# Optimization experiments

Measured on AMD Instinct MI355X. Metric: run time of the kernel, lower is better.

The kernel has to match this reference:

```python
import jax, jax.numpy as jnp
import numpy as np

G = 100000   # num graphs
N = 2000000  # num nodes
E = 4000000  # num edges (unused downstream, kept for fidelity)
D = 300      # emb_dim
L = 50       # num noise levels


def setup_inputs() -> dict:
    key = jax.random.key(0)
    ks = jax.random.split(key, 12)
    node2graph = jnp.sort(jax.random.randint(ks[0], (N,), 0, G))
    edge_index = jax.random.randint(ks[1], (2, E), 0, N)
    noise_level = jax.random.randint(ks[2], (G,), 0, L)
    molecule_repr = jax.random.normal(ks[3], (G, D), dtype=jnp.float32)
    pos_noise_pred = jax.random.normal(ks[4], (N, 3), dtype=jnp.float32)
    pos_perturbed = jax.random.normal(ks[5], (N, 3), dtype=jnp.float32)
    pos_target = jax.random.normal(ks[6], (N, 3), dtype=jnp.float32)
    s = 1.0 / np.sqrt(D)
    W1 = jax.random.uniform(ks[7], (D, D), minval=-s, maxval=s, dtype=jnp.float32)
    b1 = jax.random.uniform(ks[8], (D,), minval=-s, maxval=s, dtype=jnp.float32)
    W2 = jax.random.uniform(ks[9], (D, D), minval=-s, maxval=s, dtype=jnp.float32)
    b2 = jax.random.uniform(ks[10], (D,), minval=-s, maxval=s, dtype=jnp.float32)
    sigmas = jnp.asarray(np.exp(np.linspace(np.log(10.0), np.log(0.01), L)), dtype=jnp.float32)
    return dict(node2graph=node2graph, edge_index=edge_index, noise_level=noise_level,
                num_graphs=G, molecule_repr=molecule_repr, pos_noise_pred=pos_noise_pred,
                pos_perturbed=pos_perturbed, pos_target=pos_target,
                W1=W1, b1=b1, W2=W2, b2=b2, sigmas=sigmas)


def _score_target_riemann(pos_perturbed, pos_target, node2graph, num_graphs):
    # @torch.no_grad() branch: all scatter_mean/scatter_add indexed by node2graph
    seg_sum = lambda x: jax.ops.segment_sum(x, node2graph, num_segments=num_graphs)
    cnt = jnp.maximum(seg_sum(jnp.ones((node2graph.shape[0],), jnp.float32)), 1.0)[:, None]
    center = seg_sum(pos_target) / cnt                 # [G,3]
    p_center = seg_sum(pos_perturbed) / cnt            # [G,3]
    pos_c = pos_target - center[node2graph]            # [N,3]
    pp_c = pos_perturbed - p_center[node2graph]        # [N,3]
    # per-graph 3x3 matrices: ptp[i,j] = sum pp_i*pp_j, otp[i,j] = sum pos_c_i*pp_j
    ptp = seg_sum(pp_c[:, :, None] * pp_c[:, None, :])   # [G,3,3]
    otp = seg_sum(pos_c[:, :, None] * pp_c[:, None, :])  # [G,3,3]
    ptp_n = ptp[node2graph]                              # [N,3,3]
    otp_n = otp[node2graph]                              # [N,3,3]
    num = -2.0 * (jnp.einsum('ni,nij->nj', pp_c, ptp_n)
                  - jnp.einsum('ni,nij->nj', pos_c, otp_n))  # [N,3]
    den = (jnp.linalg.norm(ptp_n.reshape(-1, 9), axis=-1)
           + jnp.linalg.norm(otp_n.reshape(-1, 9), axis=-1))[:, None]
    return num / den


def reference(node2graph, edge_index, noise_level, num_graphs, molecule_repr,
              pos_noise_pred, pos_perturbed, pos_target, W1, b1, W2, b2, sigmas):
    edge2graph = node2graph[edge_index[0]]  # computed but unused, as in original
    used_sigmas = sigmas[noise_level][node2graph][:, None]  # [N,1]
    score_target = jax.lax.stop_gradient(
        _score_target_riemann(pos_perturbed, pos_target, node2graph, num_graphs)
    ) / used_sigmas
    pred_noise = (pos_noise_pred - pos_perturbed) * (1.0 / used_sigmas)
    per_node = jnp.sum((pred_noise - score_target) ** 2, axis=-1)  # [N]
    per_graph = jax.ops.segment_sum(per_node, node2graph, num_segments=num_graphs)
    pos_denoise = per_graph.mean()
    # noise-level prediction head: Linear -> SiLU -> Linear, CE over noise_level
    h = jax.nn.silu(molecule_repr @ W1 + b1)
    logits = h @ W2 + b2  # [G,D]
    logp = jax.nn.log_softmax(logits, axis=-1)
    ce = -jnp.take_along_axis(logp, noise_level[:, None], axis=1)[:, 0]
    loss_pred_noise = ce.mean()
    return jnp.stack([pos_denoise, loss_pred_noise])
```

## Files before the change

kernel.cpp:

```cpp
#include <hip/hip_runtime.h>
#include <math.h>


typedef __attribute__((ext_vector_type(8))) short bf16x8;
typedef __attribute__((ext_vector_type(4))) short s16x4;
typedef __attribute__((ext_vector_type(4))) float f32x4;

__device__ __forceinline__ short bt(float f) {
    return (short)(__float_as_uint(f) >> 16);
}

#define TM   32
#define DRL  300
#define DP   320
#define XS   328
#define NT   20
#define NW   5
#define KCH  10


#define NB_PREPW 800

__global__ __launch_bounds__(256)
void k_prep(const float* __restrict__ W1, const float* __restrict__ W2,
            short* __restrict__ Wb1, short* __restrict__ Wb2,
            const int* __restrict__ n2g, int* __restrict__ gs,
            int* __restrict__ ge, int N) {
    const int bid = blockIdx.x;
    const int tid = threadIdx.x;
    if (bid < NB_PREPW) {
        int id = bid * 256 + tid;
        int mat = id / (DP * DP);
        int rem = id - mat * DP * DP;
        int k = rem / DP, n = rem - (rem / DP) * DP;
        const float* W = mat ? W2 : W1;
        short* Wb = mat ? Wb2 : Wb1;
        float v = (k < DRL && n < DRL) ? W[k * DRL + n] : 0.f;
        int kc = k >> 5, kin = k & 31, quad = kin >> 3, j = kin & 7;
        int t = n >> 4, l16 = n & 15;
        Wb[(((kc * NT + t) * 64) + quad * 16 + l16) * 8 + j] = bt(v);
    } else {
        int t = (bid - NB_PREPW) * 256 + tid;
        if (t < N) {
            int g = n2g[t];
            if (t == 0     || n2g[t - 1] != g) gs[g] = t;
            if (t == N - 1 || n2g[t + 1] != g) ge[g] = t + 1;
        }
    }
}


__global__ __launch_bounds__(256, 4)
void k_main(const int* __restrict__ gs, const int* __restrict__ ge,
            const float* __restrict__ pt, const float* __restrict__ pp,
            const float* __restrict__ pnp,
            const int* __restrict__ nl, const float* __restrict__ sigmas,
            double* __restrict__ accA,
            const float* __restrict__ X,
            const short* __restrict__ Wb1, const short* __restrict__ Wb2,
            const float* __restrict__ b1, const float* __restrict__ b2,
            double* __restrict__ accC, int G) {
    __shared__ __align__(16) short Xs[TM * XS];

    const int bid = blockIdx.x;
    const int tid = threadIdx.x;
    const int t3  = bid / 3;
    const int r3  = bid - t3 * 3;

    if (r3 == 0) {
        const int tg = t3 * 256 + tid;
        const int g  = tg >> 2;
        const int j  = tg & 3;
        float q = 0.f;
        if (g < G) {
            const int s = gs[g], e = ge[g];
            const int g0 = s >> 2, g1 = (e + 3) >> 2;
            const float4* ptv = (const float4*)pt;
            const float4* ppv = (const float4*)pp;
            const float4* pnv = (const float4*)pnp;
            float st0=0,st1=0,st2=0, sp0=0,sp1=0,sp2=0;
            float m00=0,m01=0,m02=0,m11=0,m12=0,m22=0;
            float t00=0,t01=0,t02=0,t10=0,t11=0,t12=0,t20=0,t21=0,t22=0;
            for (int gg = g0 + j; gg < g1; gg += 4) {
                float4 x0 = ptv[3*gg], x1 = ptv[3*gg+1], x2 = ptv[3*gg+2];
                float4 y0 = ppv[3*gg], y1 = ppv[3*gg+1], y2 = ppv[3*gg+2];
                float A[12] = {x0.x,x0.y,x0.z,x0.w, x1.x,x1.y,x1.z,x1.w,
                               x2.x,x2.y,x2.z,x2.w};
                float B[12] = {y0.x,y0.y,y0.z,y0.w, y1.x,y1.y,y1.z,y1.w,
                               y2.x,y2.y,y2.z,y2.w};
                const int base = gg * 4;
#pragma unroll
                for (int k = 0; k < 4; ++k) {
                    const int i = base + k;
                    const bool v = (i >= s) && (i < e);
                    float a0 = v ? A[3*k+0] : 0.f;
                    float a1 = v ? A[3*k+1] : 0.f;
                    float a2 = v ? A[3*k+2] : 0.f;
                    float b0 = v ? B[3*k+0] : 0.f;
                    float b1v = v ? B[3*k+1] : 0.f;
                    float b2v = v ? B[3*k+2] : 0.f;
                    st0 += a0; st1 += a1; st2 += a2;
                    sp0 += b0; sp1 += b1v; sp2 += b2v;
                    m00 += b0*b0;  m01 += b0*b1v;  m02 += b0*b2v;
                    m11 += b1v*b1v; m12 += b1v*b2v; m22 += b2v*b2v;
                    t00 += a0*b0; t01 += a0*b1v; t02 += a0*b2v;
                    t10 += a1*b0; t11 += a1*b1v; t12 += a1*b2v;
                    t20 += a2*b0; t21 += a2*b1v; t22 += a2*b2v;
                }
            }
#define QR(x) do { x += __shfl_xor(x, 1, 64); x += __shfl_xor(x, 2, 64); } while (0)
            QR(st0); QR(st1); QR(st2); QR(sp0); QR(sp1); QR(sp2);
            QR(m00); QR(m01); QR(m02); QR(m11); QR(m12); QR(m22);
            QR(t00); QR(t01); QR(t02); QR(t10); QR(t11); QR(t12);
            QR(t20); QR(t21); QR(t22);
#undef QR
            float cnt = fmaxf((float)(e - s), 1.f);
            float ic  = 1.f / cnt;
            float c0 = st0 * ic, c1 = st1 * ic, c2 = st2 * ic;
            float d0 = sp0 * ic, d1 = sp1 * ic, d2 = sp2 * ic;
            float p00 = m00 - cnt*d0*d0, p01 = m01 - cnt*d0*d1;
            float p02 = m02 - cnt*d0*d2, p11 = m11 - cnt*d1*d1;
            float p12 = m12 - cnt*d1*d2, p22 = m22 - cnt*d2*d2;
            float o00 = t00 - cnt*c0*d0, o01 = t01 - cnt*c0*d1, o02 = t02 - cnt*c0*d2;
            float o10 = t10 - cnt*c1*d0, o11 = t11 - cnt*c1*d1, o12 = t12 - cnt*c1*d2;
            float o20 = t20 - cnt*c2*d0, o21 = t21 - cnt*c2*d1, o22 = t22 - cnt*c2*d2;
            float ptn = sqrtf(p00*p00 + p11*p11 + p22*p22 +
                              2.f*(p01*p01 + p02*p02 + p12*p12));
            float otn = sqrtf(o00*o00 + o01*o01 + o02*o02 +
                              o10*o10 + o11*o11 + o12*o12 +
                              o20*o20 + o21*o21 + o22*o22);
            float den = ptn + otn;
            float idn = (den > 0.f) ? (1.f / den) : 0.f;
            float sg  = sigmas[nl[g]];
            float is2 = 1.f / (sg * sg);
            for (int gg = g0 + j; gg < g1; gg += 4) {
                float4 x0 = ptv[3*gg], x1 = ptv[3*gg+1], x2 = ptv[3*gg+2];
                float4 y0 = ppv[3*gg], y1 = ppv[3*gg+1], y2 = ppv[3*gg+2];
                float4 z0 = pnv[3*gg], z1 = pnv[3*gg+1], z2 = pnv[3*gg+2];
                float A[12] = {x0.x,x0.y,x0.z,x0.w, x1.x,x1.y,x1.z,x1.w,
                               x2.x,x2.y,x2.z,x2.w};
                float B[12] = {y0.x,y0.y,y0.z,y0.w, y1.x,y1.y,y1.z,y1.w,
                               y2.x,y2.y,y2.z,y2.w};
                float C[12] = {z0.x,z0.y,z0.z,z0.w, z1.x,z1.y,z1.z,z1.w,
                               z2.x,z2.y,z2.z,z2.w};
                const int base = gg * 4;
#pragma unroll
                for (int k = 0; k < 4; ++k) {
                    const int i = base + k;
                    const bool v = (i >= s) && (i < e);
                    float a0 = A[3*k+0] - c0, a1 = A[3*k+1] - c1, a2 = A[3*k+2] - c2;
                    float bb0 = B[3*k+0], bb1 = B[3*k+1], bb2 = B[3*k+2];
                    float b0 = bb0 - d0, b1v = bb1 - d1, b2v = bb2 - d2;
                    float n0 = -2.f * ((b0*p00 + b1v*p01 + b2v*p02) - (a0*o00 + a1*o10 + a2*o20));
                    float n1 = -2.f * ((b0*p01 + b1v*p11 + b2v*p12) - (a0*o01 + a1*o11 + a2*o21));
                    float n2 = -2.f * ((b0*p02 + b1v*p12 + b2v*p22) - (a0*o02 + a1*o12 + a2*o22));
                    float e0 = (C[3*k+0] - bb0) - n0 * idn;
                    float e1 = (C[3*k+1] - bb1) - n1 * idn;
                    float e2 = (C[3*k+2] - bb2) - n2 * idn;
                    float contrib = (e0*e0 + e1*e1 + e2*e2) * is2;
                    q += v ? contrib : 0.f;
                }
            }
        }
        for (int o = 32; o > 0; o >>= 1) q += __shfl_down(q, o, 64);
        if ((tid & 63) == 0)
            atomicAdd(&accA[(t3 * 4 + (tid >> 6)) & 255], (double)q);
        return;
    }

    const int mid = t3 * 2 + (r3 - 1);
    const int wv   = tid >> 6;
    const int lane = tid & 63;
    const int quad = lane >> 4;
    const int l16  = lane & 15;
    const int m0   = mid * TM;
    const int tb0  = wv * NW;

    const float4* Xv = (const float4*)X;
    for (int idx = tid; idx < TM * 75; idx += 256) {
        int r = idx / 75, c = idx - r * 75;
        int gr = m0 + r;
        float4 v = {0.f, 0.f, 0.f, 0.f};
        if (gr < G) v = Xv[gr * 75 + c];
        s16x4 sv = { bt(v.x), bt(v.y), bt(v.z), bt(v.w) };
        *(s16x4*)&Xs[r * XS + c * 4] = sv;
    }
    for (int idx = tid; idx < TM * (DP - DRL); idx += 256) {
        int r = idx / (DP - DRL), c = idx - r * (DP - DRL);
        Xs[r * XS + DRL + c] = 0;
    }
    __syncthreads();

    const bf16x8* B1 = (const bf16x8*)Wb1;
    const bf16x8* B2 = (const bf16x8*)Wb2;

    f32x4 acc[2][NW];
    const f32x4 vzero = {0.f, 0.f, 0.f, 0.f};
#pragma unroll
    for (int m = 0; m < 2; ++m)
#pragma unroll
        for (int n = 0; n < NW; ++n) acc[m][n] = vzero;

#pragma unroll
    for (int kc = 0; kc < KCH; ++kc) {
        bf16x8 bv[NW];
#pragma unroll
        for (int n = 0; n < NW; ++n) bv[n] = B1[(kc * NT + tb0 + n) * 64 + lane];
        bf16x8 a0 = *(const bf16x8*)&Xs[(l16) * XS + kc * 32 + quad * 8];
        bf16x8 a1 = *(const bf16x8*)&Xs[(16 + l16) * XS + kc * 32 + quad * 8];
#pragma unroll
        for (int n = 0; n < NW; ++n) {
            acc[0][n] = __builtin_amdgcn_mfma_f32_16x16x32_bf16(a0, bv[n], acc[0][n], 0, 0, 0);
            acc[1][n] = __builtin_amdgcn_mfma_f32_16x16x32_bf16(a1, bv[n], acc[1][n], 0, 0, 0);
        }
    }
    __syncthreads();

#pragma unroll
    for (int n = 0; n < NW; ++n) {
        int col = (tb0 + n) * 16 + l16;
        float bias = (col < DRL) ? b1[col] : 0.f;
#pragma unroll
        for (int m = 0; m < 2; ++m)
#pragma unroll
            for (int r = 0; r < 4; ++r) {
                float v = acc[m][n][r] + bias;
                float h = v / (1.f + __expf(-v));
                Xs[(m * 16 + quad * 4 + r) * XS + col] = bt(h);
            }
    }
    __syncthreads();

#pragma unroll
    for (int m = 0; m < 2; ++m)
#pragma unroll
        for (int n = 0; n < NW; ++n) acc[m][n] = vzero;
#pragma unroll
    for (int kc = 0; kc < KCH; ++kc) {
        bf16x8 bv[NW];
#pragma unroll
        for (int n = 0; n < NW; ++n) bv[n] = B2[(kc * NT + tb0 + n) * 64 + lane];
        bf16x8 a0 = *(const bf16x8*)&Xs[(l16) * XS + kc * 32 + quad * 8];
        bf16x8 a1 = *(const bf16x8*)&Xs[(16 + l16) * XS + kc * 32 + quad * 8];
#pragma unroll
        for (int n = 0; n < NW; ++n) {
            acc[0][n] = __builtin_amdgcn_mfma_f32_16x16x32_bf16(a0, bv[n], acc[0][n], 0, 0, 0);
            acc[1][n] = __builtin_amdgcn_mfma_f32_16x16x32_bf16(a1, bv[n], acc[1][n], 0, 0, 0);
        }
    }
    __syncthreads();

    float* S = (float*)Xs;
    float* T = S + TM * 4;
#pragma unroll
    for (int m = 0; m < 2; ++m) {
#pragma unroll
        for (int r = 0; r < 4; ++r) {
            int row = m * 16 + quad * 4 + r;
            int grow = m0 + row;
            int ct = (grow < G) ? nl[grow] : -1;
            float sw = 0.f;
#pragma unroll
            for (int n = 0; n < NW; ++n) {
                int col = (tb0 + n) * 16 + l16;
                float lg = acc[m][n][r] + ((col < DRL) ? b2[col] : 0.f);
                if (col < DRL) sw += __expf(lg);
                if (col == ct) T[row] = lg;
            }
            for (int o = 1; o < 16; o <<= 1) sw += __shfl_xor(sw, o, 64);
            if (l16 == 0) S[row * 4 + wv] = sw;
        }
    }
    __syncthreads();
    if (tid < 64) {
        float q = 0.f;
        int row = tid;
        if (row < TM) {
            int grow = m0 + row;
            if (grow < G) {
                float ss = S[row*4+0] + S[row*4+1] + S[row*4+2] + S[row*4+3];
                q = __logf(ss) - T[row];
            }
        }
        for (int o = 32; o > 0; o >>= 1) q += __shfl_down(q, o, 64);
        if (tid == 0) atomicAdd(&accC[mid & 255], (double)q);
    }
}


__global__ void k_final(const double* __restrict__ accA,
                        const double* __restrict__ accC,
                        float* __restrict__ out, float invG) {
    int t = threadIdx.x;
    double a = accA[t] + accA[t + 64] + accA[t + 128] + accA[t + 192];
    double c = accC[t] + accC[t + 64] + accC[t + 128] + accC[t + 192];
    for (int o = 32; o > 0; o >>= 1) {
        a += __shfl_down(a, o, 64);
        c += __shfl_down(c, o, 64);
    }
    if (t == 0) {
        out[0] = (float)(a * (double)invG);
        out[1] = (float)(c * (double)invG);
    }
}


extern "C" void kernel_launch(void* const* d_in, const int* in_sizes, int n_in,
                              void* d_out, int out_size, void* d_ws, size_t ws_size,
                              hipStream_t stream) {
    const int*   n2g = (const int*)d_in[0];
    const int*   nl  = (const int*)d_in[2];
    const float* X   = (const float*)d_in[4];
    const float* pnp = (const float*)d_in[5];
    const float* pp  = (const float*)d_in[6];
    const float* pt  = (const float*)d_in[7];
    const float* W1  = (const float*)d_in[8];
    const float* b1  = (const float*)d_in[9];
    const float* W2  = (const float*)d_in[10];
    const float* b2  = (const float*)d_in[11];
    const float* sig = (const float*)d_in[12];

    const int N = in_sizes[0];
    const int G = in_sizes[2];

    double* accA = (double*)d_ws;
    double* accC = accA + 256;
    short*  Wb1  = (short*)((char*)d_ws + 4096);
    short*  Wb2  = Wb1 + DP * DP;
    int*    gs   = (int*)((char*)d_ws + 4096 + (size_t)2 * DP * DP * 2);
    int*    ge   = gs + G;

    hipMemsetAsync(d_ws, 0, 4096, stream);
    hipMemsetAsync(gs, 0, (size_t)2 * G * 4, stream);

    const int nb_bnd = (N + 255) / 256;
    const int nbg    = (4 * G + 255) / 256;
    const int nmain  = 3 * nbg;

    k_prep<<<NB_PREPW + nb_bnd, 256, 0, stream>>>(W1, W2, Wb1, Wb2,
                                                  n2g, gs, ge, N);
    k_main<<<nmain, 256, 0, stream>>>(gs, ge, pt, pp, pnp, nl, sig, accA,
                                      X, Wb1, Wb2, b1, b2, accC, G);
    k_final<<<1, 64, 0, stream>>>(accA, accC, (float*)d_out, 1.0f / (float)G);
}
```

Measured before the change: 358.7 us.

## Fuse finalize into main kernel, binary-search graph bounds, pre-convert X to bf16

Drops the two memsets and the separate final kernel. Zeroing of the accumulators moves into the prep kernel, and the final reduction is done by the last block of the main kernel through an atomic ticket. Graph start and end offsets are now found by a binary search over the sorted node2graph in the main kernel, replacing the boundary-scan pass. X is also pre-converted to padded bf16 in the prep kernel when the workspace is large enough. This cuts launches and the extra memory pass, at the cost of per-thread log(N) searches and an extra write and read of X in bf16.

```diff
diff --git a/kernel.cpp b/kernel.cpp
--- a/kernel.cpp
+++ b/kernel.cpp
@@ -17,15 +17,14 @@
 #define NT   20
 #define NW   5
 #define KCH  10
-
-
 #define NB_PREPW 800
+
 
 __global__ __launch_bounds__(256)
 void k_prep(const float* __restrict__ W1, const float* __restrict__ W2,
             short* __restrict__ Wb1, short* __restrict__ Wb2,
-            const int* __restrict__ n2g, int* __restrict__ gs,
-            int* __restrict__ ge, int N) {
+            const float* __restrict__ X, short* __restrict__ Xb,
+            double* __restrict__ accZ, int G, int nxb) {
     const int bid = blockIdx.x;
     const int tid = threadIdx.x;
     if (bid < NB_PREPW) {
@@ -39,28 +38,37 @@
         int kc = k >> 5, kin = k & 31, quad = kin >> 3, j = kin & 7;
         int t = n >> 4, l16 = n & 15;
         Wb[(((kc * NT + t) * 64) + quad * 16 + l16) * 8 + j] = bt(v);
+    } else if (bid < NB_PREPW + nxb) {
+        int id = (bid - NB_PREPW) * 256 + tid;
+        if (id < G * 80) {
+            int row = id / 80, grp = id - (id / 80) * 80;
+            float4 v = {0.f, 0.f, 0.f, 0.f};
+            if (grp < 75) v = ((const float4*)X)[row * 75 + grp];
+            s16x4 sv = { bt(v.x), bt(v.y), bt(v.z), bt(v.w) };
+            ((s16x4*)Xb)[row * 80 + grp] = sv;
+        }
     } else {
-        int t = (bid - NB_PREPW) * 256 + tid;
-        if (t < N) {
-            int g = n2g[t];
-            if (t == 0     || n2g[t - 1] != g) gs[g] = t;
-            if (t == N - 1 || n2g[t + 1] != g) ge[g] = t + 1;
-        }
+        accZ[tid] = 0.0;
+        accZ[256 + tid] = 0.0;
+        if (tid == 0) ((unsigned int*)&accZ[512])[0] = 0u;
     }
 }
 
 
 __global__ __launch_bounds__(256, 4)
-void k_main(const int* __restrict__ gs, const int* __restrict__ ge,
+void k_main(const int* __restrict__ n2g,
             const float* __restrict__ pt, const float* __restrict__ pp,
             const float* __restrict__ pnp,
             const int* __restrict__ nl, const float* __restrict__ sigmas,
-            double* __restrict__ accA,
-            const float* __restrict__ X,
+            const float* __restrict__ X, const short* __restrict__ Xb,
             const short* __restrict__ Wb1, const short* __restrict__ Wb2,
             const float* __restrict__ b1, const float* __restrict__ b2,
-            double* __restrict__ accC, int G) {
+            double* __restrict__ accA, double* __restrict__ accC,
+            unsigned int* __restrict__ ticket, float* __restrict__ out,
+            float invG, int G, int N, int nblocks, int useXb) {
     __shared__ __align__(16) short Xs[TM * XS];
+    __shared__ int lastBlk;
+    __shared__ double ax[4], cx[4];
 
     const int bid = blockIdx.x;
     const int tid = threadIdx.x;
@@ -71,9 +79,18 @@
         const int tg = t3 * 256 + tid;
         const int g  = tg >> 2;
         const int j  = tg & 3;
+        const int lane = tid & 63;
         float q = 0.f;
         if (g < G) {
-            const int s = gs[g], e = ge[g];
+            int target = g + (j & 1);
+            int lo = 0, hi = N;
+            while (lo < hi) {
+                int mid = (int)(((unsigned)lo + (unsigned)hi) >> 1);
+                if (n2g[mid] < target) lo = mid + 1; else hi = mid;
+            }
+            const int qb = lane & ~3;
+            const int s = __shfl(lo, qb + 0, 64);
+            const int e = __shfl(lo, qb + 1, 64);
             const int g0 = s >> 2, g1 = (e + 3) >> 2;
             const float4* ptv = (const float4*)pt;
             const float4* ppv = (const float4*)pp;
@@ -163,144 +180,167 @@
             }
         }
         for (int o = 32; o > 0; o >>= 1) q += __shfl_down(q, o, 64);
-        if ((tid & 63) == 0)
+        if ((tid & 63) == 0) {
             atomicAdd(&accA[(t3 * 4 + (tid >> 6)) & 255], (double)q);
-        return;
+            __threadfence();
+        }
+    } else {
+        const int mid = t3 * 2 + (r3 - 1);
+        const int wv   = tid >> 6;
+        const int lane = tid & 63;
+        const int quad = lane >> 4;
+        const int l16  = lane & 15;
+        const int m0   = mid * TM;
+        const int tb0  = wv * NW;
+
+        if (useXb) {
+            const bf16x8* Xbv = (const bf16x8*)Xb;
+#pragma unroll
+            for (int u = 0; u < 5; ++u) {
+                int idx = tid + u * 256;
+                int r = idx / 40, c8 = idx - (idx / 40) * 40;
+                int gr = m0 + r;
+                bf16x8 v = (bf16x8){0,0,0,0,0,0,0,0};
+                if (gr < G) v = Xbv[gr * 40 + c8];
+                *(bf16x8*)&Xs[r * XS + c8 * 8] = v;
+            }
+        } else {
+            const float4* Xv = (const float4*)X;
+            for (int idx = tid; idx < TM * 75; idx += 256) {
+                int r = idx / 75, c = idx - r * 75;
+                int gr = m0 + r;
+                float4 v = {0.f, 0.f, 0.f, 0.f};
+                if (gr < G) v = Xv[gr * 75 + c];
+                s16x4 sv = { bt(v.x), bt(v.y), bt(v.z), bt(v.w) };
+                *(s16x4*)&Xs[r * XS + c * 4] = sv;
+            }
+            for (int idx = tid; idx < TM * (DP - DRL); idx += 256) {
+                int r = idx / (DP - DRL), c = idx - r * (DP - DRL);
+                Xs[r * XS + DRL + c] = 0;
+            }
+        }
+        __syncthreads();
+
+        const bf16x8* B1 = (const bf16x8*)Wb1;
+        const bf16x8* B2 = (const bf16x8*)Wb2;
+
+        f32x4 acc[2][NW];
+        const f32x4 vzero = {0.f, 0.f, 0.f, 0.f};
+#pragma unroll
+        for (int m = 0; m < 2; ++m)
+#pragma unroll
+            for (int n = 0; n < NW; ++n) acc[m][n] = vzero;
+
+#pragma unroll
+        for (int kc = 0; kc < KCH; ++kc) {
+            bf16x8 bv[NW];
+#pragma unroll
+            for (int n = 0; n < NW; ++n) bv[n] = B1[(kc * NT + tb0 + n) * 64 + lane];
+            bf16x8 a0 = *(const bf16x8*)&Xs[(l16) * XS + kc * 32 + quad * 8];
+            bf16x8 a1 = *(const bf16x8*)&Xs[(16 + l16) * XS + kc * 32 + quad * 8];
+#pragma unroll
+            for (int n = 0; n < NW; ++n) {
+                acc[0][n] = __builtin_amdgcn_mfma_f32_16x16x32_bf16(a0, bv[n], acc[0][n], 0, 0, 0);
+                acc[1][n] = __builtin_amdgcn_mfma_f32_16x16x32_bf16(a1, bv[n], acc[1][n], 0, 0, 0);
+            }
+        }
+        __syncthreads();
+
+#pragma unroll
+        for (int n = 0; n < NW; ++n) {
+            int col = (tb0 + n) * 16 + l16;
+            float bias = (col < DRL) ? b1[col] : 0.f;
+#pragma unroll
+            for (int m = 0; m < 2; ++m)
+#pragma unroll
+                for (int r = 0; r < 4; ++r) {
+                    float v = acc[m][n][r] + bias;
+                    float h = v / (1.f + __expf(-v));
+                    Xs[(m * 16 + quad * 4 + r) * XS + col] = bt(h);
+                }
+        }
+        __syncthreads();
+
+#pragma unroll
+        for (int m = 0; m < 2; ++m)
+#pragma unroll
+            for (int n = 0; n < NW; ++n) acc[m][n] = vzero;
+#pragma unroll
+        for (int kc = 0; kc < KCH; ++kc) {
+            bf16x8 bv[NW];
+#pragma unroll
+            for (int n = 0; n < NW; ++n) bv[n] = B2[(kc * NT + tb0 + n) * 64 + lane];
+            bf16x8 a0 = *(const bf16x8*)&Xs[(l16) * XS + kc * 32 + quad * 8];
+            bf16x8 a1 = *(const bf16x8*)&Xs[(16 + l16) * XS + kc * 32 + quad * 8];
+#pragma unroll
+            for (int n = 0; n < NW; ++n) {
+                acc[0][n] = __builtin_amdgcn_mfma_f32_16x16x32_bf16(a0, bv[n], acc[0][n], 0, 0, 0);
+                acc[1][n] = __builtin_amdgcn_mfma_f32_16x16x32_bf16(a1, bv[n], acc[1][n], 0, 0, 0);
+            }
+        }
+        __syncthreads();
+
+        float* S = (float*)Xs;
+        float* T = S + TM * 4;
+#pragma unroll
+        for (int m = 0; m < 2; ++m) {
+#pragma unroll
+            for (int r = 0; r < 4; ++r) {
+                int row = m * 16 + quad * 4 + r;
+                int grow = m0 + row;
+                int ct = (grow < G) ? nl[grow] : -1;
+                float sw = 0.f;
+#pragma unroll
+                for (int n = 0; n < NW; ++n) {
+                    int col = (tb0 + n) * 16 + l16;
+                    float lg = acc[m][n][r] + ((col < DRL) ? b2[col] : 0.f);
+                    if (col < DRL) sw += __expf(lg);
+                    if (col == ct) T[row] = lg;
+                }
+                for (int o = 1; o < 16; o <<= 1) sw += __shfl_xor(sw, o, 64);
+                if (l16 == 0) S[row * 4 + wv] = sw;
+            }
+        }
+        __syncthreads();
+        if (tid < 64) {
+            float q = 0.f;
+            int row = tid;
+            if (row < TM) {
+                int grow = m0 + row;
+                if (grow < G) {
+                    float ss = S[row*4+0] + S[row*4+1] + S[row*4+2] + S[row*4+3];
+                    q = __logf(ss) - T[row];
+                }
+            }
+            for (int o = 32; o > 0; o >>= 1) q += __shfl_down(q, o, 64);
+            if (tid == 0) {
+                atomicAdd(&accC[mid & 255], (double)q);
+                __threadfence();
+            }
+        }
     }
 
-    const int mid = t3 * 2 + (r3 - 1);
-    const int wv   = tid >> 6;
-    const int lane = tid & 63;
-    const int quad = lane >> 4;
-    const int l16  = lane & 15;
-    const int m0   = mid * TM;
-    const int tb0  = wv * NW;
-
-    const float4* Xv = (const float4*)X;
-    for (int idx = tid; idx < TM * 75; idx += 256) {
-        int r = idx / 75, c = idx - r * 75;
-        int gr = m0 + r;
-        float4 v = {0.f, 0.f, 0.f, 0.f};
-        if (gr < G) v = Xv[gr * 75 + c];
-        s16x4 sv = { bt(v.x), bt(v.y), bt(v.z), bt(v.w) };
-        *(s16x4*)&Xs[r * XS + c * 4] = sv;
-    }
-    for (int idx = tid; idx < TM * (DP - DRL); idx += 256) {
-        int r = idx / (DP - DRL), c = idx - r * (DP - DRL);
-        Xs[r * XS + DRL + c] = 0;
+    __syncthreads();
+    if (tid == 0) {
+        unsigned int old = atomicAdd(ticket, 1u);
+        lastBlk = (old == (unsigned int)(nblocks - 1)) ? 1 : 0;
     }
     __syncthreads();
-
-    const bf16x8* B1 = (const bf16x8*)Wb1;
-    const bf16x8* B2 = (const bf16x8*)Wb2;
-
-    f32x4 acc[2][NW];
-    const f32x4 vzero = {0.f, 0.f, 0.f, 0.f};
-#pragma unroll
-    for (int m = 0; m < 2; ++m)
-#pragma unroll
-        for (int n = 0; n < NW; ++n) acc[m][n] = vzero;
-
-#pragma unroll
-    for (int kc = 0; kc < KCH; ++kc) {
-        bf16x8 bv[NW];
-#pragma unroll
-        for (int n = 0; n < NW; ++n) bv[n] = B1[(kc * NT + tb0 + n) * 64 + lane];
-        bf16x8 a0 = *(const bf16x8*)&Xs[(l16) * XS + kc * 32 + quad * 8];
-        bf16x8 a1 = *(const bf16x8*)&Xs[(16 + l16) * XS + kc * 32 + quad * 8];
-#pragma unroll
-        for (int n = 0; n < NW; ++n) {
-            acc[0][n] = __builtin_amdgcn_mfma_f32_16x16x32_bf16(a0, bv[n], acc[0][n], 0, 0, 0);
-            acc[1][n] = __builtin_amdgcn_mfma_f32_16x16x32_bf16(a1, bv[n], acc[1][n], 0, 0, 0);
-        }
-    }
-    __syncthreads();
-
-#pragma unroll
-    for (int n = 0; n < NW; ++n) {
-        int col = (tb0 + n) * 16 + l16;
-        float bias = (col < DRL) ? b1[col] : 0.f;
-#pragma unroll
-        for (int m = 0; m < 2; ++m)
-#pragma unroll
-            for (int r = 0; r < 4; ++r) {
-                float v = acc[m][n][r] + bias;
-                float h = v / (1.f + __expf(-v));
-                Xs[(m * 16 + quad * 4 + r) * XS + col] = bt(h);
-            }
-    }
-    __syncthreads();
-
-#pragma unroll
-    for (int m = 0; m < 2; ++m)
-#pragma unroll
-        for (int n = 0; n < NW; ++n) acc[m][n] = vzero;
-#pragma unroll
-    for (int kc = 0; kc < KCH; ++kc) {
-        bf16x8 bv[NW];
-#pragma unroll
-        for (int n = 0; n < NW; ++n) bv[n] = B2[(kc * NT + tb0 + n) * 64 + lane];
-        bf16x8 a0 = *(const bf16x8*)&Xs[(l16) * XS + kc * 32 + quad * 8];
-        bf16x8 a1 = *(const bf16x8*)&Xs[(16 + l16) * XS + kc * 32 + quad * 8];
-#pragma unroll
-        for (int n = 0; n < NW; ++n) {
-            acc[0][n] = __builtin_amdgcn_mfma_f32_16x16x32_bf16(a0, bv[n], acc[0][n], 0, 0, 0);
-            acc[1][n] = __builtin_amdgcn_mfma_f32_16x16x32_bf16(a1, bv[n], acc[1][n], 0, 0, 0);
-        }
-    }
-    __syncthreads();
-
-    float* S = (float*)Xs;
-    float* T = S + TM * 4;
-#pragma unroll
-    for (int m = 0; m < 2; ++m) {
-#pragma unroll
-        for (int r = 0; r < 4; ++r) {
-            int row = m * 16 + quad * 4 + r;
-            int grow = m0 + row;
-            int ct = (grow < G) ? nl[grow] : -1;
-            float sw = 0.f;
-#pragma unroll
-            for (int n = 0; n < NW; ++n) {
-                int col = (tb0 + n) * 16 + l16;
-                float lg = acc[m][n][r] + ((col < DRL) ? b2[col] : 0.f);
-                if (col < DRL) sw += __expf(lg);
-                if (col == ct) T[row] = lg;
-            }
-            for (int o = 1; o < 16; o <<= 1) sw += __shfl_xor(sw, o, 64);
-            if (l16 == 0) S[row * 4 + wv] = sw;
-        }
-    }
-    __syncthreads();
-    if (tid < 64) {
-        float q = 0.f;
-        int row = tid;
-        if (row < TM) {
-            int grow = m0 + row;
-            if (grow < G) {
-                float ss = S[row*4+0] + S[row*4+1] + S[row*4+2] + S[row*4+3];
-                q = __logf(ss) - T[row];
-            }
-        }
-        for (int o = 32; o > 0; o >>= 1) q += __shfl_down(q, o, 64);
-        if (tid == 0) atomicAdd(&accC[mid & 255], (double)q);
-    }
-}
-
-
-__global__ void k_final(const double* __restrict__ accA,
-                        const double* __restrict__ accC,
-                        float* __restrict__ out, float invG) {
-    int t = threadIdx.x;
-    double a = accA[t] + accA[t + 64] + accA[t + 128] + accA[t + 192];
-    double c = accC[t] + accC[t + 64] + accC[t + 128] + accC[t + 192];
-    for (int o = 32; o > 0; o >>= 1) {
-        a += __shfl_down(a, o, 64);
-        c += __shfl_down(c, o, 64);
-    }
-    if (t == 0) {
-        out[0] = (float)(a * (double)invG);
-        out[1] = (float)(c * (double)invG);
+    if (lastBlk) {
+        double a = atomicAdd(&accA[tid], 0.0);
+        double c = atomicAdd(&accC[tid], 0.0);
+        for (int o = 32; o > 0; o >>= 1) {
+            a += __shfl_down(a, o, 64);
+            c += __shfl_down(c, o, 64);
+        }
+        if ((tid & 63) == 0) { ax[tid >> 6] = a; cx[tid >> 6] = c; }
+        __syncthreads();
+        if (tid == 0) {
+            double A2 = ax[0] + ax[1] + ax[2] + ax[3];
+            double C2 = cx[0] + cx[1] + cx[2] + cx[3];
+            out[0] = (float)(A2 * (double)invG);
+            out[1] = (float)(C2 * (double)invG);
+        }
     }
 }
 
@@ -323,23 +363,23 @@
     const int N = in_sizes[0];
     const int G = in_sizes[2];
 
-    double* accA = (double*)d_ws;
-    double* accC = accA + 256;
-    short*  Wb1  = (short*)((char*)d_ws + 4096);
-    short*  Wb2  = Wb1 + DP * DP;
-    int*    gs   = (int*)((char*)d_ws + 4096 + (size_t)2 * DP * DP * 2);
-    int*    ge   = gs + G;
-
-    hipMemsetAsync(d_ws, 0, 4096, stream);
-    hipMemsetAsync(gs, 0, (size_t)2 * G * 4, stream);
-
-    const int nb_bnd = (N + 255) / 256;
-    const int nbg    = (4 * G + 255) / 256;
-    const int nmain  = 3 * nbg;
-
-    k_prep<<<NB_PREPW + nb_bnd, 256, 0, stream>>>(W1, W2, Wb1, Wb2,
-                                                  n2g, gs, ge, N);
-    k_main<<<nmain, 256, 0, stream>>>(gs, ge, pt, pp, pnp, nl, sig, accA,
-                                      X, Wb1, Wb2, b1, b2, accC, G);
-    k_final<<<1, 64, 0, stream>>>(accA, accC, (float*)d_out, 1.0f / (float)G);
+    double*       accA   = (double*)d_ws;
+    double*       accC   = accA + 256;
+    unsigned int* ticket = (unsigned int*)(accA + 512);
+    short*        Wb1    = (short*)((char*)d_ws + 8192);
+    short*        Wb2    = Wb1 + DP * DP;
+    short*        Xb     = Wb2 + DP * DP;
+    const size_t need = 8192 + (size_t)2 * DP * DP * 2 + (size_t)G * DP * 2;
+    const int useXb = (ws_size >= need) ? 1 : 0;
+    const int nxb = useXb ? (G * 80 + 255) / 256 : 0;
+
+    const int nbg   = (4 * G + 255) / 256;
+    const int nmain = 3 * nbg;
+
+    k_prep<<<NB_PREPW + nxb + 1, 256, 0, stream>>>(W1, W2, Wb1, Wb2,
+                                                   X, Xb, accA, G, nxb);
+    k_main<<<nmain, 256, 0, stream>>>(n2g, pt, pp, pnp, nl, sig, X, Xb,
+                                      Wb1, Wb2, b1, b2, accA, accC, ticket,
+                                      (float*)d_out, 1.0f / (float)G,
+                                      G, N, nmain, useXb);
 }
```

Result: slower. 692.9 us (+93.2%).
